# Performance work log

Hardware: AMD Instinct MI355X
Metric: run time of the kernel (lower is better)

Reference implementation:

```python
import jax, jax.numpy as jnp
import numpy as np

N_NODES = 100000
N_EDGES = 3200000
N_FEAT = 512
N_HID = 256
N_CLASS = 40
K_HOPS = 10


def setup_inputs() -> dict:
    key = jax.random.key(0)
    ks = jax.random.split(key, 8)
    feature = jax.random.normal(ks[0], (N_NODES, N_FEAT), dtype=jnp.float32)
    edge_row = jax.random.randint(ks[1], (N_EDGES,), 0, N_NODES, dtype=jnp.int32)
    edge_col = jax.random.randint(ks[2], (N_EDGES,), 0, N_NODES, dtype=jnp.int32)
    edge_weight = jax.random.uniform(ks[3], (N_EDGES,), dtype=jnp.float32)
    W1 = jax.random.normal(ks[4], (N_FEAT, N_HID), dtype=jnp.float32) * (1.0 / np.sqrt(N_FEAT))
    b1 = jnp.zeros((N_HID,), dtype=jnp.float32)
    W2 = jax.random.normal(ks[5], (N_HID, N_CLASS), dtype=jnp.float32) * (1.0 / np.sqrt(N_HID))
    b2 = jnp.zeros((N_CLASS,), dtype=jnp.float32)
    Wa = jax.random.normal(ks[6], (N_CLASS, 1), dtype=jnp.float32) * (1.0 / np.sqrt(N_CLASS))
    ba = jnp.zeros((1,), dtype=jnp.float32)
    return {"feature": feature, "edge_row": edge_row, "edge_col": edge_col,
            "edge_weight": edge_weight, "W1": W1, "b1": b1, "W2": W2, "b2": b2,
            "Wa": Wa, "ba": ba}


def reference(feature, edge_row, edge_col, edge_weight, W1, b1, W2, b2, Wa, ba):
    # eval mode: dropout is identity
    x = jax.nn.relu(feature @ W1 + b1)          # [N, H]
    x = x @ W2 + b2                              # [N, C]
    # k-hop sparse propagation: out[i] = sum_e w_e * x[col_e] for row_e == i
    xs = [x]
    for _ in range(K_HOPS):
        x = jax.ops.segment_sum(edge_weight[:, None] * x[edge_col], edge_row,
                                num_segments=N_NODES)
        xs.append(x)
    xs = jnp.stack(xs, axis=1)                   # [N, K+1, C]
    score = jax.nn.sigmoid(jnp.squeeze(xs @ Wa + ba, -1))  # [N, K+1]
    out = jnp.einsum('nk,nkc->nc', score, xs)    # attention-weighted hop sum
    return jax.nn.log_softmax(out, axis=1)
```

## Files before the change

kernel.cpp:

```cpp
#include <hip/hip_runtime.h>
#include <math.h>

#define N_NODES 100000
#define N_EDGES 3200000
#define N_FEAT  512
#define N_HID   256
#define N_CLASS 40
#define K_HOPS  10

#define CAP        80

#define BIN_SHIFT  11
#define NBIN       49
#define NBIN_PAD   56
#define BINCAP     68000
#define CHUNK1     4096
#define CHUNK2     4096
#define CPB2       17

typedef __attribute__((ext_vector_type(8))) short short8;
typedef __attribute__((ext_vector_type(8))) unsigned short ushort8v;
typedef __attribute__((ext_vector_type(4))) float float4v;
typedef unsigned long long u64;

__device__ inline short f2bf(float f)
{
    union { float f; unsigned u; } v; v.f = f;
    unsigned r = v.u + 0x7FFF + ((v.u >> 16) & 1);
    return (short)(r >> 16);
}

__device__ inline float bf2f(unsigned short u)
{
    union { unsigned u; float f; } v; v.u = (unsigned)u << 16;
    return v.f;
}

__device__ inline short8 cvt8(const float4& a, const float4& b)
{
    union { unsigned u[4]; short8 s; } r;
    asm("v_cvt_pk_bf16_f32 %0, %1, %2" : "=v"(r.u[0]) : "v"(a.x), "v"(a.y));
    asm("v_cvt_pk_bf16_f32 %0, %1, %2" : "=v"(r.u[1]) : "v"(a.z), "v"(a.w));
    asm("v_cvt_pk_bf16_f32 %0, %1, %2" : "=v"(r.u[2]) : "v"(b.x), "v"(b.y));
    asm("v_cvt_pk_bf16_f32 %0, %1, %2" : "=v"(r.u[3]) : "v"(b.z), "v"(b.w));
    return r.s;
}

__global__ void pack_w1(const float* __restrict__ W1, short* __restrict__ W1p)
{
    const int id = blockIdx.x * 256 + threadIdx.x;
    const int kb = id >> 8, n = id & 255;
    short tmp[32];
#pragma unroll
    for (int kl = 0; kl < 32; ++kl)
        tmp[kl] = f2bf(W1[(size_t)(kb * 32 + kl) * N_HID + n]);
    short8* dst = (short8*)&W1p[id * 32];
#pragma unroll
    for (int j = 0; j < 4; ++j) dst[j] = *(short8*)&tmp[j * 8];
}

__global__ void pack_w2(const float* __restrict__ W2, short* __restrict__ W2p)
{
    const int id = blockIdx.x * 256 + threadIdx.x;
    if (id >= 8 * 48) return;
    const int kb = id / 48, n = id % 48;
    short tmp[32];
#pragma unroll
    for (int kl = 0; kl < 32; ++kl)
        tmp[kl] = (n < N_CLASS) ? f2bf(W2[(size_t)(kb * 32 + kl) * N_CLASS + n]) : (short)0;
    short8* dst = (short8*)&W2p[id * 32];
#pragma unroll
    for (int j = 0; j < 4; ++j) dst[j] = *(short8*)&tmp[j * 8];
}

__global__ __launch_bounds__(256, 2) void mlp_mfma(
    const float* __restrict__ feat, const short* __restrict__ W1p,
    const float* __restrict__ b1, const short* __restrict__ W2p,
    const float* __restrict__ b2, const float* __restrict__ Wa,
    const float* __restrict__ ba,
    unsigned short* __restrict__ x0, float* __restrict__ acc_out)
{
    __shared__ __align__(16) short smem[64 * 264];
    short (*Hs)[264] = (short(*)[264])smem;

    const int t    = threadIdx.x;
    const int wave = t >> 6;
    const int lane = t & 63;
    const int q    = lane >> 4;
    const int m    = lane & 15;
    const int n0   = blockIdx.x * 64;
    const int RB   = wave >> 1;
    const int CB   = wave & 1;

    const float* ap[2];
#pragma unroll
    for (int rt = 0; rt < 2; ++rt) {
        int r = n0 + RB * 32 + rt * 16 + m;
        if (r > N_NODES - 1) r = N_NODES - 1;
        ap[rt] = &feat[(size_t)r * N_FEAT + q * 8];
    }
    const short* bp = &W1p[(CB * 128 + m) * 32 + q * 8];

    float4v acc[2][8];
#pragma unroll
    for (int rt = 0; rt < 2; ++rt)
#pragma unroll
        for (int ct = 0; ct < 8; ++ct) acc[rt][ct] = (float4v)0.f;

    float4 A0[3][2], A1[3][2];
    short8 Bp[2][8];

#pragma unroll
    for (int s = 0; s < 2; ++s)
#pragma unroll
        for (int rt = 0; rt < 2; ++rt) {
            A0[s][rt] = *(const float4*)(ap[rt] + s * 32);
            A1[s][rt] = *(const float4*)(ap[rt] + s * 32 + 4);
        }
#pragma unroll
    for (int ct = 0; ct < 8; ++ct)
        Bp[0][ct] = *(const short8*)(bp + (ct * 16) * 32);

#pragma unroll
    for (int kb = 0; kb < 16; ++kb) {
        const int sA_ld = (kb + 2) % 3;
        const int sB_ld = (kb + 1) & 1;
        const int sA    = kb % 3;
        const int sB    = kb & 1;
        if (kb + 2 < 16) {
#pragma unroll
            for (int rt = 0; rt < 2; ++rt) {
                A0[sA_ld][rt] = *(const float4*)(ap[rt] + (kb + 2) * 32);
                A1[sA_ld][rt] = *(const float4*)(ap[rt] + (kb + 2) * 32 + 4);
            }
        }
        if (kb + 1 < 16) {
#pragma unroll
            for (int ct = 0; ct < 8; ++ct)
                Bp[sB_ld][ct] = *(const short8*)(bp + ((kb + 1) * 256 + ct * 16) * 32);
        }
        short8 a8[2];
#pragma unroll
        for (int rt = 0; rt < 2; ++rt) a8[rt] = cvt8(A0[sA][rt], A1[sA][rt]);
#pragma unroll
        for (int rt = 0; rt < 2; ++rt)
#pragma unroll
            for (int ct = 0; ct < 8; ++ct)
                acc[rt][ct] = __builtin_amdgcn_mfma_f32_16x16x32_bf16(
                    a8[rt], Bp[sB][ct], acc[rt][ct], 0, 0, 0);
    }

#pragma unroll
    for (int rt = 0; rt < 2; ++rt)
#pragma unroll
        for (int ct = 0; ct < 8; ++ct) {
            const int col = CB * 128 + ct * 16 + m;
            const float bias = b1[col];
            const float4v d = acc[rt][ct];
#pragma unroll
            for (int r = 0; r < 4; ++r) {
                const int row = RB * 32 + rt * 16 + q * 4 + r;
                Hs[row][col] = f2bf(fmaxf(d[r] + bias, 0.f));
            }
        }
    __syncthreads();

    float4v acc2[3];
#pragma unroll
    for (int ct = 0; ct < 3; ++ct) acc2[ct] = (float4v)0.f;
#pragma unroll
    for (int kb = 0; kb < 8; ++kb) {
        const short8 a2 = *(const short8*)&Hs[wave * 16 + m][kb * 32 + q * 8];
#pragma unroll
        for (int ct = 0; ct < 3; ++ct) {
            const int off = (kb * 48 + ct * 16 + m) * 32 + q * 8;
            const short8 b2f = *(const short8*)&W2p[off];
            acc2[ct] = __builtin_amdgcn_mfma_f32_16x16x32_bf16(a2, b2f, acc2[ct], 0, 0, 0);
        }
    }

    float val[3][4];
#pragma unroll
    for (int ct = 0; ct < 3; ++ct) {
        const int col = ct * 16 + m;
        const bool cok = col < N_CLASS;
        const float bias = cok ? b2[col] : 0.f;
#pragma unroll
        for (int r = 0; r < 4; ++r) val[ct][r] = acc2[ct][r] + bias;
        if (cok) {
#pragma unroll
            for (int r = 0; r < 4; ++r) {
                const int row = n0 + wave * 16 + q * 4 + r;
                if (row < N_NODES)
                    x0[(size_t)row * N_CLASS + col] = (unsigned short)f2bf(val[ct][r]);
            }
        }
    }
    float part[4];
#pragma unroll
    for (int r = 0; r < 4; ++r) {
        float p = 0.f;
#pragma unroll
        for (int ct = 0; ct < 3; ++ct) {
            const int col = ct * 16 + m;
            if (col < N_CLASS) p += val[ct][r] * Wa[col];
        }
        part[r] = p;
    }
#pragma unroll
    for (int o = 1; o <= 8; o <<= 1)
#pragma unroll
        for (int r = 0; r < 4; ++r) part[r] += __shfl_xor(part[r], o);
    const float bb = ba[0];
#pragma unroll
    for (int r = 0; r < 4; ++r) {
        const int row = n0 + wave * 16 + q * 4 + r;
        if (row < N_NODES) {
            const float sc = 1.f / (1.f + expf(-(part[r] + bb)));
#pragma unroll
            for (int ct = 0; ct < 3; ++ct) {
                const int col = ct * 16 + m;
                if (col < N_CLASS)
                    acc_out[(size_t)row * N_CLASS + col] = sc * val[ct][r];
            }
        }
    }
}

__global__ __launch_bounds__(256) void bin_kernel(
    const int* __restrict__ erow, const int* __restrict__ ecol,
    const float* __restrict__ ew, int* __restrict__ bin_cursor,
    u64* __restrict__ bins)
{
    __shared__ __align__(16) u64 recs[CHUNK1];
    __shared__ int hist[NBIN], h2[NBIN], lbase[NBIN], adj[NBIN];

    const int t     = threadIdx.x;
    const int cbase = blockIdx.x * CHUNK1;
    const int e0    = cbase + t * 16;
    const bool has  = e0 < N_EDGES;
    const int chunk_n = min(CHUNK1, N_EDGES - cbase);

    for (int i = t; i < NBIN; i += 256) { hist[i] = 0; h2[i] = 0; }
    __syncthreads();

    int   rows[16], cols[16], w15[16];
    if (has) {
#pragma unroll
        for (int qv = 0; qv < 4; ++qv) {
            const int4   r = *(const int4*)&erow[e0 + qv * 4];
            const int4   c = *(const int4*)&ecol[e0 + qv * 4];
            const float4 w = *(const float4*)&ew[e0 + qv * 4];
            rows[qv*4+0]=r.x; rows[qv*4+1]=r.y; rows[qv*4+2]=r.z; rows[qv*4+3]=r.w;
            cols[qv*4+0]=c.x; cols[qv*4+1]=c.y; cols[qv*4+2]=c.z; cols[qv*4+3]=c.w;
            const float wf[4] = {w.x, w.y, w.z, w.w};
#pragma unroll
            for (int j = 0; j < 4; ++j) {
                int v = (int)(wf[j] * 32767.f + 0.5f);
                w15[qv*4+j] = (v > 32767) ? 32767 : v;
            }
        }
#pragma unroll
        for (int j = 0; j < 16; ++j)
            atomicAdd(&hist[rows[j] >> BIN_SHIFT], 1);
    }
    __syncthreads();

    if (t == 0) {
        int run = 0;
        for (int b = 0; b < NBIN; ++b) { lbase[b] = run; run += hist[b]; }
    }
    __syncthreads();
    if (t < NBIN) {
        const int g = atomicAdd(&bin_cursor[t], hist[t]);
        adj[t] = g - lbase[t];
    }
    __syncthreads();

    if (has) {
#pragma unroll
        for (int j = 0; j < 16; ++j) {
            const int b = rows[j] >> BIN_SHIFT;
            const int p = lbase[b] + atomicAdd(&h2[b], 1);
            recs[p] = ((u64)w15[j] << 34) | ((u64)rows[j] << 17) | (u64)cols[j];
        }
    }
    __syncthreads();

    for (int i = t; i < chunk_n; i += 256) {
        const u64 r   = recs[i];
        const int row = (int)((r >> 17) & 0x1FFFF);
        const int b   = row >> BIN_SHIFT;
        const int di  = adj[b] + i;
        if (di < BINCAP)
            bins[(size_t)b * BINCAP + di] = r;
    }
}

__global__ __launch_bounds__(256) void scatter_bins(
    const int* __restrict__ bin_cursor, const u64* __restrict__ bins,
    int* __restrict__ cnt, unsigned int* __restrict__ ebuck)
{
    const int b = blockIdx.x % NBIN_PAD;
    if (b >= NBIN) return;
    const int chunk = blockIdx.x / NBIN_PAD;
    int n = bin_cursor[b];
    if (n > BINCAP) n = BINCAP;
    const int start = chunk * CHUNK2;
    if (start >= n) return;
    const u64* src = &bins[(size_t)b * BINCAP];

#pragma unroll
    for (int j = 0; j < 16; ++j) {
        const int idx = start + j * 256 + threadIdx.x;
        if (idx < n) {
            const u64 r   = src[idx];
            const int col = (int)(r & 0x1FFFF);
            const int row = (int)((r >> 17) & 0x1FFFF);
            const unsigned rec = ((unsigned)(r >> 34) << 17) | (unsigned)col;
            const int pos = atomicAdd(&cnt[row], 1);
            if (pos < CAP)
                ebuck[(size_t)row * CAP + pos] = rec;
        }
    }
}

template <bool LAST>
__global__ __launch_bounds__(256) void hop_kernel(
    const int* __restrict__ cnt, const unsigned int* __restrict__ ebuck,
    const unsigned short* __restrict__ xin,
    unsigned short* __restrict__ xout, float* __restrict__ acc,
    const float* __restrict__ Wa, const float* __restrict__ ba,
    float* __restrict__ out)
{
    const int lane = threadIdx.x & 63;
    const int row  = blockIdx.x * 4 + (threadIdx.x >> 6);
    if (row >= N_NODES) return;
    const int  slot = lane >> 3;
    const int  l    = lane & 7;
    const bool act  = l < 5;

    int n = cnt[row];
    if (n > CAP) n = CAP;
    const size_t ebase = (size_t)row * CAP;

    unsigned rec_a = (lane < n) ? ebuck[ebase + lane] : 0u;

    float s[8];
#pragma unroll
    for (int j = 0; j < 8; ++j) s[j] = 0.f;

    const int nmain = (n < 64) ? n : 64;
    for (int e = 0; e < nmain; e += 8) {
        const unsigned r = __shfl(rec_a, e + slot);
        const int   col  = (int)(r & 0x1FFFFu);
        const float w    = (float)(r >> 17) * (1.f / 32767.f);
        if (act) {
            const ushort8v v = *(const ushort8v*)&xin[(size_t)col * N_CLASS + l * 8];
#pragma unroll
            for (int j = 0; j < 8; ++j) s[j] += w * bf2f(v[j]);
        }
    }
    for (int e = 64; e < n; e += 8) {
        const int ee = e + slot;
        unsigned r = 0u;
        if (ee < n) r = ebuck[ebase + ee];
        const int   col = (int)(r & 0x1FFFFu);
        const float w   = (float)(r >> 17) * (1.f / 32767.f);
        if (act) {
            const ushort8v v = *(const ushort8v*)&xin[(size_t)col * N_CLASS + l * 8];
#pragma unroll
            for (int j = 0; j < 8; ++j) s[j] += w * bf2f(v[j]);
        }
    }

#pragma unroll
    for (int o = 8; o <= 32; o <<= 1)
#pragma unroll
        for (int j = 0; j < 8; ++j) s[j] += __shfl_xor(s[j], o);

    float tq = 0.f;
    if (act) {
#pragma unroll
        for (int j = 0; j < 8; ++j) tq += s[j] * Wa[l * 8 + j];
    }
#pragma unroll
    for (int o = 1; o <= 4; o <<= 1) tq += __shfl_xor(tq, o);
    const float z  = tq + ba[0];
    const float sc = 1.f / (1.f + expf(-z));

    const bool wr = act && slot == 0;
    if (!LAST) {
        if (wr) {
            ushort8v ov;
#pragma unroll
            for (int j = 0; j < 8; ++j) ov[j] = (unsigned short)f2bf(s[j]);
            *(ushort8v*)&xout[(size_t)row * N_CLASS + l * 8] = ov;

            float4* ap0 = (float4*)&acc[(size_t)row * N_CLASS + l * 8];
            float4 a0 = ap0[0];
            float4 a1 = ap0[1];
            a0.x += sc * s[0]; a0.y += sc * s[1]; a0.z += sc * s[2]; a0.w += sc * s[3];
            a1.x += sc * s[4]; a1.y += sc * s[5]; a1.z += sc * s[6]; a1.w += sc * s[7];
            ap0[0] = a0;
            ap0[1] = a1;
        }
    } else {
        float av[8];
        float mxl = -INFINITY;
        if (wr) {
            const float4* ap0 = (const float4*)&acc[(size_t)row * N_CLASS + l * 8];
            const float4 a0 = ap0[0];
            const float4 a1 = ap0[1];
            av[0] = a0.x + sc * s[0]; av[1] = a0.y + sc * s[1];
            av[2] = a0.z + sc * s[2]; av[3] = a0.w + sc * s[3];
            av[4] = a1.x + sc * s[4]; av[5] = a1.y + sc * s[5];
            av[6] = a1.z + sc * s[6]; av[7] = a1.w + sc * s[7];
#pragma unroll
            for (int j = 0; j < 8; ++j) mxl = fmaxf(mxl, av[j]);
        }
        float mx = mxl;
#pragma unroll
        for (int o = 1; o <= 4; o <<= 1) mx = fmaxf(mx, __shfl_xor(mx, o));
        float se = 0.f;
        if (wr) {
#pragma unroll
            for (int j = 0; j < 8; ++j) se += expf(av[j] - mx);
        }
#pragma unroll
        for (int o = 1; o <= 4; o <<= 1) se += __shfl_xor(se, o);
        if (wr) {
            const float ls = logf(se);
            float4 o0, o1;
            o0.x = av[0] - mx - ls; o0.y = av[1] - mx - ls;
            o0.z = av[2] - mx - ls; o0.w = av[3] - mx - ls;
            o1.x = av[4] - mx - ls; o1.y = av[5] - mx - ls;
            o1.z = av[6] - mx - ls; o1.w = av[7] - mx - ls;
            float4* op = (float4*)&out[(size_t)row * N_CLASS + l * 8];
            op[0] = o0;
            op[1] = o1;
        }
    }
}

extern "C" void kernel_launch(void* const* d_in, const int* in_sizes, int n_in,
                              void* d_out, int out_size, void* d_ws, size_t ws_size,
                              hipStream_t stream)
{
    (void)in_sizes; (void)n_in; (void)out_size; (void)ws_size;
    const float* feat = (const float*)d_in[0];
    const int*   erow = (const int*)d_in[1];
    const int*   ecol = (const int*)d_in[2];
    const float* ew   = (const float*)d_in[3];
    const float* W1   = (const float*)d_in[4];
    const float* b1   = (const float*)d_in[5];
    const float* W2   = (const float*)d_in[6];
    const float* b2   = (const float*)d_in[7];
    const float* Wa   = (const float*)d_in[8];
    const float* ba   = (const float*)d_in[9];
    float* out = (float*)d_out;

    char* ws = (char*)d_ws;
    size_t off = 0;
    auto take = [&](size_t bytes) -> char* {
        char* p = ws + off;
        off += (bytes + 255) & ~(size_t)255;
        return p;
    };
    unsigned short* xb0 = (unsigned short*)take((size_t)N_NODES * N_CLASS * 2 + 64);
    unsigned short* xb1 = (unsigned short*)take((size_t)N_NODES * N_CLASS * 2 + 64);
    float*        acc   = (float*)take((size_t)N_NODES * N_CLASS * 4);
    int*          cnt   = (int*)take((size_t)N_NODES * 4);
    int*          bcur  = (int*)take((size_t)NBIN_PAD * 4);
    short*        W1p   = (short*)take((size_t)N_FEAT * N_HID * 2);
    short*        W2p   = (short*)take((size_t)N_HID * 48 * 2);
    unsigned int* ebuck = (unsigned int*)take((size_t)N_NODES * CAP * 4);
    u64*          bins  = (u64*)take((size_t)NBIN * BINCAP * 8);

    hipMemsetAsync(cnt, 0, (size_t)N_NODES * 4, stream);
    hipMemsetAsync(bcur, 0, (size_t)NBIN_PAD * 4, stream);

    pack_w1<<<16, 256, 0, stream>>>(W1, W1p);
    pack_w2<<<2, 256, 0, stream>>>(W2, W2p);
    mlp_mfma<<<(N_NODES + 63) / 64, 256, 0, stream>>>(feat, W1p, b1, W2p, b2,
                                                      Wa, ba, xb0, acc);

    const int nchunk1 = (N_EDGES + CHUNK1 - 1) / CHUNK1;
    bin_kernel<<<nchunk1, 256, 0, stream>>>(erow, ecol, ew, bcur, bins);
    scatter_bins<<<NBIN_PAD * CPB2, 256, 0, stream>>>(bcur, bins, cnt, ebuck);

    const unsigned short* xin = xb0;
    unsigned short* xout = xb1;
    for (int k = 0; k < K_HOPS - 1; ++k) {
        hop_kernel<false><<<N_NODES / 4, 256, 0, stream>>>(
            cnt, ebuck, xin, xout, acc, Wa, ba, out);
        unsigned short* tmp = (unsigned short*)xin;
        xin  = xout;
        xout = tmp;
    }
    hop_kernel<true><<<N_NODES / 4, 256, 0, stream>>>(
        cnt, ebuck, xin, xout, acc, Wa, ba, out);
}
```

Baseline: 1.200 ms.

## Stage MLP feature tiles via direct-to-LDS loads and batch hop gathers

```diff
diff --git a/kernel.cpp b/kernel.cpp
--- a/kernel.cpp
+++ b/kernel.cpp
@@ -46,6 +46,13 @@
     return r.s;
 }
 
+__device__ inline void gload_lds16(const void* g, void* l)
+{
+    __builtin_amdgcn_global_load_lds(
+        (const __attribute__((address_space(1))) unsigned*)g,
+        (__attribute__((address_space(3))) unsigned*)l, 16, 0, 0);
+}
+
 __global__ void pack_w1(const float* __restrict__ W1, short* __restrict__ W1p)
 {
     const int id = blockIdx.x * 256 + threadIdx.x;
@@ -73,7 +80,7 @@
     for (int j = 0; j < 4; ++j) dst[j] = *(short8*)&tmp[j * 8];
 }
 
-__global__ __launch_bounds__(256, 2) void mlp_mfma(
+__global__ __launch_bounds__(256) void mlp_mfma(
     const float* __restrict__ feat, const short* __restrict__ W1p,
     const float* __restrict__ b1, const short* __restrict__ W2p,
     const float* __restrict__ b2, const float* __restrict__ Wa,
@@ -81,6 +88,7 @@
     unsigned short* __restrict__ x0, float* __restrict__ acc_out)
 {
     __shared__ __align__(16) short smem[64 * 264];
+    char* abase      = (char*)smem;
     short (*Hs)[264] = (short(*)[264])smem;
 
     const int t    = threadIdx.x;
@@ -89,80 +97,71 @@
     const int q    = lane >> 4;
     const int m    = lane & 15;
     const int n0   = blockIdx.x * 64;
-    const int RB   = wave >> 1;
-    const int CB   = wave & 1;
-
-    const float* ap[2];
-#pragma unroll
-    for (int rt = 0; rt < 2; ++rt) {
-        int r = n0 + RB * 32 + rt * 16 + m;
+    const int colbase = wave * 64;
+
+    const int gg = (lane & 7) ^ ((lane >> 3) & 7);
+    const float* sp[2];
+#pragma unroll
+    for (int s2 = 0; s2 < 2; ++s2) {
+        int r = n0 + wave * 16 + s2 * 8 + (lane >> 3);
         if (r > N_NODES - 1) r = N_NODES - 1;
-        ap[rt] = &feat[(size_t)r * N_FEAT + q * 8];
-    }
-    const short* bp = &W1p[(CB * 128 + m) * 32 + q * 8];
-
-    float4v acc[2][8];
-#pragma unroll
-    for (int rt = 0; rt < 2; ++rt)
-#pragma unroll
-        for (int ct = 0; ct < 8; ++ct) acc[rt][ct] = (float4v)0.f;
-
-    float4 A0[3][2], A1[3][2];
-    short8 Bp[2][8];
-
-#pragma unroll
-    for (int s = 0; s < 2; ++s)
-#pragma unroll
-        for (int rt = 0; rt < 2; ++rt) {
-            A0[s][rt] = *(const float4*)(ap[rt] + s * 32);
-            A1[s][rt] = *(const float4*)(ap[rt] + s * 32 + 4);
-        }
-#pragma unroll
-    for (int ct = 0; ct < 8; ++ct)
-        Bp[0][ct] = *(const short8*)(bp + (ct * 16) * 32);
-
-#pragma unroll
+        sp[s2] = &feat[(size_t)r * N_FEAT + gg * 4];
+    }
+    char* lbase = abase + wave * 2048;
+
+    float4v acc[4][4];
+#pragma unroll
+    for (int i = 0; i < 4; ++i)
+#pragma unroll
+        for (int j = 0; j < 4; ++j) acc[i][j] = (float4v)0.f;
+
+    gload_lds16(sp[0], lbase);
+    gload_lds16(sp[1], lbase + 1024);
+    __syncthreads();
+
     for (int kb = 0; kb < 16; ++kb) {
-        const int sA_ld = (kb + 2) % 3;
-        const int sB_ld = (kb + 1) & 1;
-        const int sA    = kb % 3;
-        const int sB    = kb & 1;
-        if (kb + 2 < 16) {
-#pragma unroll
-            for (int rt = 0; rt < 2; ++rt) {
-                A0[sA_ld][rt] = *(const float4*)(ap[rt] + (kb + 2) * 32);
-                A1[sA_ld][rt] = *(const float4*)(ap[rt] + (kb + 2) * 32 + 4);
+        if (kb < 15) {
+            char* lb = lbase + ((kb + 1) & 1) * 8192;
+            gload_lds16(sp[0] + (kb + 1) * 32, lb);
+            gload_lds16(sp[1] + (kb + 1) * 32, lb + 1024);
+        }
+        const char* ab = abase + (kb & 1) * 8192;
+        short8 af[4], bfr[4];
+#pragma unroll
+        for (int rt = 0; rt < 4; ++rt) {
+            const int rowL = rt * 16 + m;
+            const float4 fa = *(const float4*)(ab + rowL * 128 + ((2 * q)     ^ (m & 7)) * 16);
+            const float4 fb = *(const float4*)(ab + rowL * 128 + ((2 * q + 1) ^ (m & 7)) * 16);
+            af[rt] = cvt8(fa, fb);
+        }
+#pragma unroll
+        for (int ct = 0; ct < 4; ++ct) {
+            const int off = (kb * 256 + colbase + ct * 16 + m) * 32 + q * 8;
+            bfr[ct] = *(const short8*)&W1p[off];
+        }
+#pragma unroll
+        for (int rt = 0; rt < 4; ++rt)
+#pragma unroll
+            for (int ct = 0; ct < 4; ++ct)
+                acc[rt][ct] = __builtin_amdgcn_mfma_f32_16x16x32_bf16(
+                    af[rt], bfr[ct], acc[rt][ct], 0, 0, 0);
+        __syncthreads();
+    }
+
+#pragma unroll
+    for (int ct = 0; ct < 4; ++ct) {
+        const int col = colbase + ct * 16 + m;
+        const float bias = b1[col];
+#pragma unroll
+        for (int rt = 0; rt < 4; ++rt) {
+            const float4v d = acc[rt][ct];
+#pragma unroll
+            for (int r = 0; r < 4; ++r) {
+                const float hv = fmaxf(d[r] + bias, 0.f);
+                Hs[rt * 16 + q * 4 + r][col] = f2bf(hv);
             }
         }
-        if (kb + 1 < 16) {
-#pragma unroll
-            for (int ct = 0; ct < 8; ++ct)
-                Bp[sB_ld][ct] = *(const short8*)(bp + ((kb + 1) * 256 + ct * 16) * 32);
-        }
-        short8 a8[2];
-#pragma unroll
-        for (int rt = 0; rt < 2; ++rt) a8[rt] = cvt8(A0[sA][rt], A1[sA][rt]);
-#pragma unroll
-        for (int rt = 0; rt < 2; ++rt)
-#pragma unroll
-            for (int ct = 0; ct < 8; ++ct)
-                acc[rt][ct] = __builtin_amdgcn_mfma_f32_16x16x32_bf16(
-                    a8[rt], Bp[sB][ct], acc[rt][ct], 0, 0, 0);
-    }
-
-#pragma unroll
-    for (int rt = 0; rt < 2; ++rt)
-#pragma unroll
-        for (int ct = 0; ct < 8; ++ct) {
-            const int col = CB * 128 + ct * 16 + m;
-            const float bias = b1[col];
-            const float4v d = acc[rt][ct];
-#pragma unroll
-            for (int r = 0; r < 4; ++r) {
-                const int row = RB * 32 + rt * 16 + q * 4 + r;
-                Hs[row][col] = f2bf(fmaxf(d[r] + bias, 0.f));
-            }
-        }
+    }
     __syncthreads();
 
     float4v acc2[3];
@@ -346,31 +345,45 @@
 
     unsigned rec_a = (lane < n) ? ebuck[ebase + lane] : 0u;
 
+    const int nit = ((n < 64 ? n : 64) + 7) >> 3;
+
+    float    w[8];
+    ushort8v v[8];
+#pragma unroll
+    for (int it = 0; it < 8; ++it) {
+        if (it < nit) {
+            const unsigned r = __shfl(rec_a, it * 8 + slot);
+            w[it] = (float)(r >> 17) * (1.f / 32767.f);
+            const int col = (int)(r & 0x1FFFFu);
+            if (act)
+                v[it] = *(const ushort8v*)&xin[(size_t)col * N_CLASS + l * 8];
+        }
+    }
+
     float s[8];
 #pragma unroll
     for (int j = 0; j < 8; ++j) s[j] = 0.f;
 
-    const int nmain = (n < 64) ? n : 64;
-    for (int e = 0; e < nmain; e += 8) {
-        const unsigned r = __shfl(rec_a, e + slot);
-        const int   col  = (int)(r & 0x1FFFFu);
-        const float w    = (float)(r >> 17) * (1.f / 32767.f);
-        if (act) {
-            const ushort8v v = *(const ushort8v*)&xin[(size_t)col * N_CLASS + l * 8];
-#pragma unroll
-            for (int j = 0; j < 8; ++j) s[j] += w * bf2f(v[j]);
-        }
-    }
+#pragma unroll
+    for (int it = 0; it < 8; ++it) {
+        if (it < nit) {
+            if (act) {
+#pragma unroll
+                for (int j = 0; j < 8; ++j) s[j] += w[it] * bf2f(v[it][j]);
+            }
+        }
+    }
+
     for (int e = 64; e < n; e += 8) {
         const int ee = e + slot;
         unsigned r = 0u;
         if (ee < n) r = ebuck[ebase + ee];
         const int   col = (int)(r & 0x1FFFFu);
-        const float w   = (float)(r >> 17) * (1.f / 32767.f);
+        const float wt  = (float)(r >> 17) * (1.f / 32767.f);
         if (act) {
-            const ushort8v v = *(const ushort8v*)&xin[(size_t)col * N_CLASS + l * 8];
-#pragma unroll
-            for (int j = 0; j < 8; ++j) s[j] += w * bf2f(v[j]);
+            const ushort8v vt = *(const ushort8v*)&xin[(size_t)col * N_CLASS + l * 8];
+#pragma unroll
+            for (int j = 0; j < 8; ++j) s[j] += wt * bf2f(vt[j]);
         }
     }
 
```

Result: faster. 1.162 ms (-3.2%).
